# Optimization experiments

Hardware: AMD Instinct MI355X
Metric: run time of the kernel (lower is better)

## Reference

```python
import jax, jax.numpy as jnp
import numpy as np

ALPHA = 1.0


def setup_inputs() -> dict:
    key = jax.random.key(0)
    k1, k2 = jax.random.split(key)
    N, K, D = 131072, 512, 512
    inputs = jax.random.normal(k1, (N, D), dtype=jnp.float32)
    # xavier-uniform style init for clusters
    limit = float(np.sqrt(6.0 / (K + D)))
    clusters = jax.random.uniform(k2, (K, D), dtype=jnp.float32, minval=-limit, maxval=limit)
    return {"inputs": inputs, "clusters": clusters}


def reference(inputs, clusters):
    # (same math as sum((x[:,None,:]-c)**2, -1), without the N x K x D intermediate)
    x2 = jnp.sum(inputs * inputs, axis=1, keepdims=True)          # [N, 1]
    c2 = jnp.sum(clusters * clusters, axis=1)[None, :]            # [1, K]
    d2 = jnp.maximum(x2 + c2 - 2.0 * (inputs @ clusters.T), 0.0)  # [N, K]
    q = 1.0 / (1.0 + d2 / ALPHA)
    q = q ** ((ALPHA + 1.0) / 2.0)
    return q / jnp.sum(q, axis=1, keepdims=True)
```

## Files before the change

kernel.cpp:

```cpp
#include <hip/hip_runtime.h>
#include <stdint.h>

#define NPTS 131072
#define DIM  512
#define KC   512
#define BM   64
#define BK   32
#define NKT  16

typedef float f32x16 __attribute__((ext_vector_type(16)));
typedef float f32x4  __attribute__((ext_vector_type(4)));
typedef short bf16x8 __attribute__((ext_vector_type(8)));
typedef short bf16x4 __attribute__((ext_vector_type(4)));

__device__ __forceinline__ short f2bf(float f) {
  union { float f; unsigned u; } v; v.f = f;
  unsigned r = v.u + 0x7FFFu + ((v.u >> 16) & 1u);
  return (short)(r >> 16);
}

__device__ __forceinline__ bf16x8 pack8(f32x4 a, f32x4 b) {
  bf16x8 p;
  p[0] = f2bf(a.x); p[1] = f2bf(a.y); p[2] = f2bf(a.z); p[3] = f2bf(a.w);
  p[4] = f2bf(b.x); p[5] = f2bf(b.y); p[6] = f2bf(b.z); p[7] = f2bf(b.w);
  return p;
}

__device__ __forceinline__ bf16x4 pack4(f32x4 a) {
  bf16x4 p;
  p[0] = f2bf(a.x); p[1] = f2bf(a.y); p[2] = f2bf(a.z); p[3] = f2bf(a.w);
  return p;
}

__device__ __forceinline__ float sq4(f32x4 a) {
  return a.x*a.x + a.y*a.y + a.z*a.z + a.w*a.w;
}

__device__ __forceinline__ void gload_lds16(const short* g, short* l) {
  __builtin_amdgcn_global_load_lds(
      (const __attribute__((address_space(1))) unsigned int*)g,
      (__attribute__((address_space(3))) unsigned int*)l, 16, 0, 0);
}

__global__ void dec_pack(const float* __restrict__ C, short* __restrict__ Bp,
                         float* __restrict__ c2) {
  const int n    = blockIdx.x;
  const int lane = threadIdx.x;
  const float* src = C + (size_t)n * DIM + lane * 8;
  f32x4 v0 = *(const f32x4*)src;
  f32x4 v1 = *(const f32x4*)(src + 4);
  float s = sq4(v0) + sq4(v1);
  #pragma unroll
  for (int m = 1; m < 64; m <<= 1) s += __shfl_xor(s, m, 64);
  if (lane == 0) c2[n] = s;
  const int kt = lane >> 2;
  const int st = (lane >> 1) & 1;
  const int hh = lane & 1;
  const int wn = n >> 7, nt = (n >> 5) & 3, r = n & 31;
  const size_t slot =
      (((size_t)(kt * 2 + st) * 4 + wn) * 4 + nt) * 64 + hh * 32 + r;
  *(bf16x8*)(Bp + slot * 8) = pack8(v0, v1);
}

__global__ __launch_bounds__(512, 4)
void dec_main(const float* __restrict__ X, const short* __restrict__ Bp,
              const float* __restrict__ c2g, float* __restrict__ out) {
  __shared__ short Bbuf[2][KC * BK];
  __shared__ short Abuf[2][2 * 2 * BM * 8];
  __shared__ float x2sh[BM];
  __shared__ float part[4][BM];
  __shared__ float rowinv[BM];

  const int tid  = threadIdx.x;
  const int lane = tid & 63;
  const int wave = tid >> 6;
  const int wm   = wave >> 2;
  const int wn   = wave & 3;
  const int l31  = lane & 31;
  const int h    = lane >> 5;
  const int row0 = blockIdx.x * BM;

  const int arow = tid >> 3;
  const int ac   = tid & 7;
  const float* aptr = X + (size_t)(row0 + arow) * DIM + ac * 4;
  const int awoff = (((ac >> 2) * 2 + ((ac >> 1) & 1)) * BM + arow) * 8 +
                    (ac & 1) * 4;

  const short* bsrc = Bp + tid * 8;

  f32x16 acc[4];
  #pragma unroll
  for (int nt = 0; nt < 4; ++nt) acc[nt] = (f32x16)0.f;
  float x2a = 0.f;

  {
    #pragma unroll
    for (int sw = 0; sw < 4; ++sw)
      gload_lds16(bsrc + sw * 4096, &Bbuf[0][sw * 4096 + tid * 8]);
    f32x4 a0 = *(const f32x4*)(aptr);
    x2a += sq4(a0);
    *(bf16x4*)&Abuf[0][awoff] = pack4(a0);
  }
  f32x4 av_w = *(const f32x4*)(aptr + 1 * BK);
  f32x4 av_p = *(const f32x4*)(aptr + 2 * BK);
  __syncthreads();

  for (int kt = 0; kt < NKT; ++kt) {
    const int cur = kt & 1, nxt = cur ^ 1;

    if (kt + 1 < NKT) {
      const int kpre = (kt + 3 < NKT) ? (kt + 3) : (NKT - 1);
      f32x4 av_n = *(const f32x4*)(aptr + kpre * BK);
      #pragma unroll
      for (int sw = 0; sw < 4; ++sw)
        gload_lds16(bsrc + (size_t)(kt + 1) * 16384 + sw * 4096,
                    &Bbuf[nxt][sw * 4096 + tid * 8]);
      x2a += sq4(av_w);
      *(bf16x4*)&Abuf[nxt][awoff] = pack4(av_w);
      av_w = av_p;
      av_p = av_n;
    }

    #pragma unroll
    for (int s = 0; s < 2; ++s) {
      bf16x8 af = *(const bf16x8*)
          &Abuf[cur][((s * 2 + h) * BM + wm * 32 + l31) * 8];
      bf16x8 bfr[4];
      #pragma unroll
      for (int nt = 0; nt < 4; ++nt)
        bfr[nt] = *(const bf16x8*)
            &Bbuf[cur][((s * 4 + wn) * 4 + nt) * 512 + lane * 8];
      #pragma unroll
      for (int nt = 0; nt < 4; ++nt)
        acc[nt] = __builtin_amdgcn_mfma_f32_32x32x16_bf16(
            af, bfr[nt], acc[nt], 0, 0, 0);
    }

    __syncthreads();
  }

  x2a += __shfl_xor(x2a, 1, 64);
  x2a += __shfl_xor(x2a, 2, 64);
  x2a += __shfl_xor(x2a, 4, 64);
  if ((tid & 7) == 0) x2sh[arow] = x2a;
  __syncthreads();

  float c2v[4];
  #pragma unroll
  for (int nt = 0; nt < 4; ++nt) c2v[nt] = c2g[wn * 128 + nt * 32 + l31];

  float srow[16];
  #pragma unroll
  for (int r = 0; r < 16; ++r) {
    const int mloc = (r & 3) + 8 * (r >> 2) + 4 * h;
    const float x2m = x2sh[wm * 32 + mloc];
    float s = 0.f;
    #pragma unroll
    for (int nt = 0; nt < 4; ++nt) {
      float d2 = fmaxf(x2m + c2v[nt] - 2.f * acc[nt][r], 0.f);
      float q = __builtin_amdgcn_rcpf(1.f + d2);
      acc[nt][r] = q;
      s += q;
    }
    #pragma unroll
    for (int msk = 1; msk < 32; msk <<= 1) s += __shfl_xor(s, msk, 64);
    srow[r] = s;
  }

  if (l31 == 0) {
    #pragma unroll
    for (int r = 0; r < 16; ++r)
      part[wn][wm * 32 + (r & 3) + 8 * (r >> 2) + 4 * h] = srow[r];
  }
  __syncthreads();
  if (tid < BM)
    rowinv[tid] = __builtin_amdgcn_rcpf(part[0][tid] + part[1][tid] +
                                        part[2][tid] + part[3][tid]);
  __syncthreads();

  #pragma unroll
  for (int r = 0; r < 16; ++r) {
    const int row = wm * 32 + (r & 3) + 8 * (r >> 2) + 4 * h;
    const float iv = rowinv[row];
    float* o = out + (size_t)(row0 + row) * KC + wn * 128 + l31;
    #pragma unroll
    for (int nt = 0; nt < 4; ++nt)
      o[nt * 32] = acc[nt][r] * iv;
  }
}

extern "C" void kernel_launch(void* const* d_in, const int* in_sizes, int n_in,
                              void* d_out, int out_size, void* d_ws, size_t ws_size,
                              hipStream_t stream) {
  const float* X = (const float*)d_in[0];
  const float* C = (const float*)d_in[1];
  float* out = (float*)d_out;

  short* Bp = (short*)d_ws;
  float* c2 = (float*)((char*)d_ws + (size_t)KC * DIM * 2);

  dec_pack<<<KC, 64, 0, stream>>>(C, Bp, c2);
  dec_main<<<NPTS / BM, 512, 0, stream>>>(X, Bp, c2, out);
}
```

Before: 177.5 us.

## Use per-wave private A staging and direct global B loads, removing block barriers

Each wave now loads and converts its own 32-row slice of X into a wave-private LDS double buffer. It also reads packed cluster fragments straight from global memory into registers, so the shared B LDS tile and the per-k-step __syncthreads are gone. Row norms are kept in registers and broadcast with shuffles instead of going through shared memory. The costs are redundant X loads across the four waves that share a wm, more global/L2 traffic for B, more registers, and occupancy lowered to 2 blocks per SM. There is also no wave-level barrier between the LDS write and the read of the next buffer, which relies on in-order wave execution.

```diff
diff --git a/kernel.cpp b/kernel.cpp
--- a/kernel.cpp
+++ b/kernel.cpp
@@ -1,45 +1,44 @@
 #include <hip/hip_runtime.h>
+#include <hip/hip_bf16.h>
 #include <stdint.h>
 
 #define NPTS 131072
 #define DIM  512
 #define KC   512
 #define BM   64
-#define BK   32
 #define NKT  16
 
 typedef float f32x16 __attribute__((ext_vector_type(16)));
 typedef float f32x4  __attribute__((ext_vector_type(4)));
 typedef short bf16x8 __attribute__((ext_vector_type(8)));
-typedef short bf16x4 __attribute__((ext_vector_type(4)));
+
+__device__ __forceinline__ float sq4(f32x4 a) {
+  return a.x*a.x + a.y*a.y + a.z*a.z + a.w*a.w;
+}
+
+__device__ __forceinline__ bf16x8 pack8c(f32x4 a, f32x4 b) {
+  bf16x8 r;
+  float v[8] = {a.x, a.y, a.z, a.w, b.x, b.y, b.z, b.w};
+  #pragma unroll
+  for (int i = 0; i < 4; ++i) {
+    __hip_bfloat162 t = __float22bfloat162_rn(make_float2(v[2*i], v[2*i+1]));
+    union { __hip_bfloat162 h; short s[2]; } u; u.h = t;
+    r[2*i]   = u.s[0];
+    r[2*i+1] = u.s[1];
+  }
+  return r;
+}
 
 __device__ __forceinline__ short f2bf(float f) {
   union { float f; unsigned u; } v; v.f = f;
   unsigned r = v.u + 0x7FFFu + ((v.u >> 16) & 1u);
   return (short)(r >> 16);
 }
-
 __device__ __forceinline__ bf16x8 pack8(f32x4 a, f32x4 b) {
   bf16x8 p;
   p[0] = f2bf(a.x); p[1] = f2bf(a.y); p[2] = f2bf(a.z); p[3] = f2bf(a.w);
   p[4] = f2bf(b.x); p[5] = f2bf(b.y); p[6] = f2bf(b.z); p[7] = f2bf(b.w);
   return p;
-}
-
-__device__ __forceinline__ bf16x4 pack4(f32x4 a) {
-  bf16x4 p;
-  p[0] = f2bf(a.x); p[1] = f2bf(a.y); p[2] = f2bf(a.z); p[3] = f2bf(a.w);
-  return p;
-}
-
-__device__ __forceinline__ float sq4(f32x4 a) {
-  return a.x*a.x + a.y*a.y + a.z*a.z + a.w*a.w;
-}
-
-__device__ __forceinline__ void gload_lds16(const short* g, short* l) {
-  __builtin_amdgcn_global_load_lds(
-      (const __attribute__((address_space(1))) unsigned int*)g,
-      (__attribute__((address_space(3))) unsigned int*)l, 16, 0, 0);
 }
 
 __global__ void dec_pack(const float* __restrict__ C, short* __restrict__ Bp,
@@ -62,12 +61,10 @@
   *(bf16x8*)(Bp + slot * 8) = pack8(v0, v1);
 }
 
-__global__ __launch_bounds__(512, 4)
+__global__ __launch_bounds__(512, 2)
 void dec_main(const float* __restrict__ X, const short* __restrict__ Bp,
               const float* __restrict__ c2g, float* __restrict__ out) {
-  __shared__ short Bbuf[2][KC * BK];
-  __shared__ short Abuf[2][2 * 2 * BM * 8];
-  __shared__ float x2sh[BM];
+  __shared__ short Apriv[8][2][1024];
   __shared__ float part[4][BM];
   __shared__ float rowinv[BM];
 
@@ -80,70 +77,86 @@
   const int h    = lane >> 5;
   const int row0 = blockIdx.x * BM;
 
-  const int arow = tid >> 3;
-  const int ac   = tid & 7;
-  const float* aptr = X + (size_t)(row0 + arow) * DIM + ac * 4;
-  const int awoff = (((ac >> 2) * 2 + ((ac >> 1) & 1)) * BM + arow) * 8 +
-                    (ac & 1) * 4;
-
-  const short* bsrc = Bp + tid * 8;
+  const float* aptr =
+      X + (size_t)(row0 + wm * 32 + (lane >> 2)) * DIM + (lane & 3) * 8;
+  const short* bB = Bp + wn * 2048 + lane * 8;
+  const int awoff = (lane & 3) * 256 + (lane >> 2) * 8;
 
   f32x16 acc[4];
   #pragma unroll
   for (int nt = 0; nt < 4; ++nt) acc[nt] = (f32x16)0.f;
-  float x2a = 0.f;
+  float x2s[2] = {0.f, 0.f};
 
   {
-    #pragma unroll
-    for (int sw = 0; sw < 4; ++sw)
-      gload_lds16(bsrc + sw * 4096, &Bbuf[0][sw * 4096 + tid * 8]);
-    f32x4 a0 = *(const f32x4*)(aptr);
-    x2a += sq4(a0);
-    *(bf16x4*)&Abuf[0][awoff] = pack4(a0);
-  }
-  f32x4 av_w = *(const f32x4*)(aptr + 1 * BK);
-  f32x4 av_p = *(const f32x4*)(aptr + 2 * BK);
-  __syncthreads();
-
+    f32x4 a0[2][2];
+    #pragma unroll
+    for (int j = 0; j < 2; ++j) {
+      a0[j][0] = *(const f32x4*)(aptr + j * 8192);
+      a0[j][1] = *(const f32x4*)(aptr + j * 8192 + 4);
+    }
+    #pragma unroll
+    for (int j = 0; j < 2; ++j) {
+      x2s[j] += sq4(a0[j][0]) + sq4(a0[j][1]);
+      *(bf16x8*)&Apriv[wave][0][awoff + j * 128] = pack8c(a0[j][0], a0[j][1]);
+    }
+  }
+  f32x4 aC[2][2];
+  #pragma unroll
+  for (int j = 0; j < 2; ++j) {
+    aC[j][0] = *(const f32x4*)(aptr + 32 + j * 8192);
+    aC[j][1] = *(const f32x4*)(aptr + 32 + j * 8192 + 4);
+  }
+
+  #pragma unroll 2
   for (int kt = 0; kt < NKT; ++kt) {
-    const int cur = kt & 1, nxt = cur ^ 1;
+    const int cur = kt & 1;
+
+    f32x4 aN[2][2];
+    if (kt + 2 < NKT) {
+      #pragma unroll
+      for (int j = 0; j < 2; ++j) {
+        aN[j][0] = *(const f32x4*)(aptr + (kt + 2) * 32 + j * 8192);
+        aN[j][1] = *(const f32x4*)(aptr + (kt + 2) * 32 + j * 8192 + 4);
+      }
+    }
+
+    bf16x8 bq[2][4];
+    #pragma unroll
+    for (int s = 0; s < 2; ++s)
+      #pragma unroll
+      for (int nt = 0; nt < 4; ++nt)
+        bq[s][nt] = *(const bf16x8*)(bB + kt * 16384 + s * 8192 + nt * 512);
 
     if (kt + 1 < NKT) {
-      const int kpre = (kt + 3 < NKT) ? (kt + 3) : (NKT - 1);
-      f32x4 av_n = *(const f32x4*)(aptr + kpre * BK);
-      #pragma unroll
-      for (int sw = 0; sw < 4; ++sw)
-        gload_lds16(bsrc + (size_t)(kt + 1) * 16384 + sw * 4096,
-                    &Bbuf[nxt][sw * 4096 + tid * 8]);
-      x2a += sq4(av_w);
-      *(bf16x4*)&Abuf[nxt][awoff] = pack4(av_w);
-      av_w = av_p;
-      av_p = av_n;
+      #pragma unroll
+      for (int j = 0; j < 2; ++j) {
+        x2s[j] += sq4(aC[j][0]) + sq4(aC[j][1]);
+        *(bf16x8*)&Apriv[wave][cur ^ 1][awoff + j * 128] =
+            pack8c(aC[j][0], aC[j][1]);
+      }
     }
 
     #pragma unroll
     for (int s = 0; s < 2; ++s) {
-      bf16x8 af = *(const bf16x8*)
-          &Abuf[cur][((s * 2 + h) * BM + wm * 32 + l31) * 8];
-      bf16x8 bfr[4];
-      #pragma unroll
-      for (int nt = 0; nt < 4; ++nt)
-        bfr[nt] = *(const bf16x8*)
-            &Bbuf[cur][((s * 4 + wn) * 4 + nt) * 512 + lane * 8];
+      bf16x8 af = *(const bf16x8*)&Apriv[wave][cur][(s * 2 + h) * 256 + l31 * 8];
       #pragma unroll
       for (int nt = 0; nt < 4; ++nt)
         acc[nt] = __builtin_amdgcn_mfma_f32_32x32x16_bf16(
-            af, bfr[nt], acc[nt], 0, 0, 0);
-    }
-
-    __syncthreads();
-  }
-
-  x2a += __shfl_xor(x2a, 1, 64);
-  x2a += __shfl_xor(x2a, 2, 64);
-  x2a += __shfl_xor(x2a, 4, 64);
-  if ((tid & 7) == 0) x2sh[arow] = x2a;
-  __syncthreads();
+            af, bq[s][nt], acc[nt], 0, 0, 0);
+    }
+
+    #pragma unroll
+    for (int j = 0; j < 2; ++j) {
+      aC[j][0] = aN[j][0];
+      aC[j][1] = aN[j][1];
+    }
+  }
+
+  #pragma unroll
+  for (int j = 0; j < 2; ++j) {
+    x2s[j] += __shfl_xor(x2s[j], 1, 64);
+    x2s[j] += __shfl_xor(x2s[j], 2, 64);
+  }
 
   float c2v[4];
   #pragma unroll
@@ -153,7 +166,7 @@
   #pragma unroll
   for (int r = 0; r < 16; ++r) {
     const int mloc = (r & 3) + 8 * (r >> 2) + 4 * h;
-    const float x2m = x2sh[wm * 32 + mloc];
+    const float x2m = __shfl(x2s[mloc >> 4], (mloc & 15) * 4, 64);
     float s = 0.f;
     #pragma unroll
     for (int nt = 0; nt < 4; ++nt) {
```

Result: slower. 216.0 us (+21.7%).

## Pre-pack inputs to bf16 MFMA layout and drop LDS staging in main GEMM

Applied to the files above, without the earlier changes.

Adds a separate kernel that converts X to bf16 in the MFMA fragment layout and computes row norms. The main kernel then reads A and B fragments directly from global memory into registers, with no LDS double buffering or barriers in the k-loop. This is meant to remove LDS traffic and synchronisation from the GEMM loop. The cost is an extra pass over X, a large bf16 workspace write, and more global/L2 reads of B per wave. The old kernel is kept as a fallback when the workspace is too small.

```diff
diff --git a/kernel.cpp b/kernel.cpp
--- a/kernel.cpp
+++ b/kernel.cpp
@@ -1,45 +1,44 @@
 #include <hip/hip_runtime.h>
+#include <hip/hip_bf16.h>
 #include <stdint.h>
 
 #define NPTS 131072
 #define DIM  512
 #define KC   512
 #define BM   64
-#define BK   32
 #define NKT  16
 
 typedef float f32x16 __attribute__((ext_vector_type(16)));
 typedef float f32x4  __attribute__((ext_vector_type(4)));
 typedef short bf16x8 __attribute__((ext_vector_type(8)));
-typedef short bf16x4 __attribute__((ext_vector_type(4)));
+
+__device__ __forceinline__ float sq4(f32x4 a) {
+  return a.x*a.x + a.y*a.y + a.z*a.z + a.w*a.w;
+}
+
+__device__ __forceinline__ bf16x8 pack8c(f32x4 a, f32x4 b) {
+  bf16x8 r;
+  float v[8] = {a.x, a.y, a.z, a.w, b.x, b.y, b.z, b.w};
+  #pragma unroll
+  for (int i = 0; i < 4; ++i) {
+    __hip_bfloat162 t = __float22bfloat162_rn(make_float2(v[2*i], v[2*i+1]));
+    union { __hip_bfloat162 h; short s[2]; } u; u.h = t;
+    r[2*i]   = u.s[0];
+    r[2*i+1] = u.s[1];
+  }
+  return r;
+}
 
 __device__ __forceinline__ short f2bf(float f) {
   union { float f; unsigned u; } v; v.f = f;
   unsigned r = v.u + 0x7FFFu + ((v.u >> 16) & 1u);
   return (short)(r >> 16);
 }
-
 __device__ __forceinline__ bf16x8 pack8(f32x4 a, f32x4 b) {
   bf16x8 p;
   p[0] = f2bf(a.x); p[1] = f2bf(a.y); p[2] = f2bf(a.z); p[3] = f2bf(a.w);
   p[4] = f2bf(b.x); p[5] = f2bf(b.y); p[6] = f2bf(b.z); p[7] = f2bf(b.w);
   return p;
-}
-
-__device__ __forceinline__ bf16x4 pack4(f32x4 a) {
-  bf16x4 p;
-  p[0] = f2bf(a.x); p[1] = f2bf(a.y); p[2] = f2bf(a.z); p[3] = f2bf(a.w);
-  return p;
-}
-
-__device__ __forceinline__ float sq4(f32x4 a) {
-  return a.x*a.x + a.y*a.y + a.z*a.z + a.w*a.w;
-}
-
-__device__ __forceinline__ void gload_lds16(const short* g, short* l) {
-  __builtin_amdgcn_global_load_lds(
-      (const __attribute__((address_space(1))) unsigned int*)g,
-      (__attribute__((address_space(3))) unsigned int*)l, 16, 0, 0);
 }
 
 __global__ void dec_pack(const float* __restrict__ C, short* __restrict__ Bp,
@@ -62,12 +61,31 @@
   *(bf16x8*)(Bp + slot * 8) = pack8(v0, v1);
 }
 
-__global__ __launch_bounds__(512, 4)
-void dec_main(const float* __restrict__ X, const short* __restrict__ Bp,
-              const float* __restrict__ c2g, float* __restrict__ out) {
-  __shared__ short Bbuf[2][KC * BK];
-  __shared__ short Abuf[2][2 * 2 * BM * 8];
-  __shared__ float x2sh[BM];
+__global__ __launch_bounds__(256)
+void dec_packx(const float* __restrict__ X, short* __restrict__ Xp,
+               float* __restrict__ x2g) {
+  const int g    = blockIdx.x * 4 + (threadIdx.x >> 6);
+  const int lane = threadIdx.x & 63;
+  const int h    = lane >> 5;
+  const int r    = lane & 31;
+  const float* src = X + (size_t)(g * 32 + r) * DIM + h * 8;
+  short* dst = Xp + (size_t)g * 16384 + lane * 8;
+  float x2 = 0.f;
+  #pragma unroll 4
+  for (int ks = 0; ks < 32; ++ks) {
+    f32x4 lo = *(const f32x4*)(src + ks * 16);
+    f32x4 hi = *(const f32x4*)(src + ks * 16 + 4);
+    x2 += sq4(lo) + sq4(hi);
+    *(bf16x8*)(dst + ks * 512) = pack8c(lo, hi);
+  }
+  x2 += __shfl_xor(x2, 32, 64);
+  if (lane < 32) x2g[g * 32 + r] = x2;
+}
+
+__global__ __launch_bounds__(512)
+void dec_main2(const short* __restrict__ Xp, const short* __restrict__ Bp,
+               const float* __restrict__ c2g, const float* __restrict__ x2g,
+               float* __restrict__ out) {
   __shared__ float part[4][BM];
   __shared__ float rowinv[BM];
 
@@ -79,13 +97,124 @@
   const int l31  = lane & 31;
   const int h    = lane >> 5;
   const int row0 = blockIdx.x * BM;
+  const int g    = blockIdx.x * 2 + wm;
+
+  const short* aB = Xp + (size_t)g * 16384 + lane * 8;
+  const short* bB = Bp + wn * 2048 + lane * 8;
+
+  f32x16 acc[4];
+  #pragma unroll
+  for (int nt = 0; nt < 4; ++nt) acc[nt] = (f32x16)0.f;
+
+  bf16x8 aF[2][2];
+  #pragma unroll
+  for (int s = 0; s < 2; ++s)
+    aF[0][s] = *(const bf16x8*)(aB + s * 512);
+
+  #pragma unroll
+  for (int kt = 0; kt < NKT; ++kt) {
+    bf16x8 bF[2][4];
+    #pragma unroll
+    for (int s = 0; s < 2; ++s)
+      #pragma unroll
+      for (int nt = 0; nt < 4; ++nt)
+        bF[s][nt] = *(const bf16x8*)(bB + kt * 16384 + s * 8192 + nt * 512);
+
+    if (kt + 1 < NKT) {
+      #pragma unroll
+      for (int s = 0; s < 2; ++s)
+        aF[(kt + 1) & 1][s] =
+            *(const bf16x8*)(aB + (kt + 1) * 1024 + s * 512);
+    }
+
+    #pragma unroll
+    for (int s = 0; s < 2; ++s)
+      #pragma unroll
+      for (int nt = 0; nt < 4; ++nt)
+        acc[nt] = __builtin_amdgcn_mfma_f32_32x32x16_bf16(
+            aF[kt & 1][s], bF[s][nt], acc[nt], 0, 0, 0);
+  }
+
+  const float x2v = x2g[row0 + wm * 32 + l31];
+  float c2v[4];
+  #pragma unroll
+  for (int nt = 0; nt < 4; ++nt) c2v[nt] = c2g[wn * 128 + nt * 32 + l31];
+
+  float srow[16];
+  #pragma unroll
+  for (int r = 0; r < 16; ++r) {
+    const int mloc = (r & 3) + 8 * (r >> 2) + 4 * h;
+    const float x2m = __shfl(x2v, mloc, 64);
+    float s = 0.f;
+    #pragma unroll
+    for (int nt = 0; nt < 4; ++nt) {
+      float d2 = fmaxf(x2m + c2v[nt] - 2.f * acc[nt][r], 0.f);
+      float q = __builtin_amdgcn_rcpf(1.f + d2);
+      acc[nt][r] = q;
+      s += q;
+    }
+    #pragma unroll
+    for (int msk = 1; msk < 32; msk <<= 1) s += __shfl_xor(s, msk, 64);
+    srow[r] = s;
+  }
+
+  if (l31 == 0) {
+    #pragma unroll
+    for (int r = 0; r < 16; ++r)
+      part[wn][wm * 32 + (r & 3) + 8 * (r >> 2) + 4 * h] = srow[r];
+  }
+  __syncthreads();
+  if (tid < BM)
+    rowinv[tid] = __builtin_amdgcn_rcpf(part[0][tid] + part[1][tid] +
+                                        part[2][tid] + part[3][tid]);
+  __syncthreads();
+
+  #pragma unroll
+  for (int r = 0; r < 16; ++r) {
+    const int row = wm * 32 + (r & 3) + 8 * (r >> 2) + 4 * h;
+    const float iv = rowinv[row];
+    float* o = out + (size_t)(row0 + row) * KC + wn * 128 + l31;
+    #pragma unroll
+    for (int nt = 0; nt < 4; ++nt)
+      o[nt * 32] = acc[nt][r] * iv;
+  }
+}
+
+typedef short bf16x4 __attribute__((ext_vector_type(4)));
+__device__ __forceinline__ bf16x4 pack4(f32x4 a) {
+  bf16x4 p;
+  p[0] = f2bf(a.x); p[1] = f2bf(a.y); p[2] = f2bf(a.z); p[3] = f2bf(a.w);
+  return p;
+}
+__device__ __forceinline__ void gload_lds16(const short* g, short* l) {
+  __builtin_amdgcn_global_load_lds(
+      (const __attribute__((address_space(1))) unsigned int*)g,
+      (__attribute__((address_space(3))) unsigned int*)l, 16, 0, 0);
+}
+
+__global__ __launch_bounds__(512, 4)
+void dec_main_fb(const float* __restrict__ X, const short* __restrict__ Bp,
+                 const float* __restrict__ c2g, float* __restrict__ out) {
+  __shared__ short Bbuf[2][KC * 32];
+  __shared__ short Abuf[2][2 * 2 * BM * 8];
+  __shared__ float x2sh[BM];
+  __shared__ float part[4][BM];
+  __shared__ float rowinv[BM];
+
+  const int tid  = threadIdx.x;
+  const int lane = tid & 63;
+  const int wave = tid >> 6;
+  const int wm   = wave >> 2;
+  const int wn   = wave & 3;
+  const int l31  = lane & 31;
+  const int h    = lane >> 5;
+  const int row0 = blockIdx.x * BM;
 
   const int arow = tid >> 3;
   const int ac   = tid & 7;
   const float* aptr = X + (size_t)(row0 + arow) * DIM + ac * 4;
   const int awoff = (((ac >> 2) * 2 + ((ac >> 1) & 1)) * BM + arow) * 8 +
                     (ac & 1) * 4;
-
   const short* bsrc = Bp + tid * 8;
 
   f32x16 acc[4];
@@ -101,16 +230,15 @@
     x2a += sq4(a0);
     *(bf16x4*)&Abuf[0][awoff] = pack4(a0);
   }
-  f32x4 av_w = *(const f32x4*)(aptr + 1 * BK);
-  f32x4 av_p = *(const f32x4*)(aptr + 2 * BK);
+  f32x4 av_w = *(const f32x4*)(aptr + 32);
+  f32x4 av_p = *(const f32x4*)(aptr + 64);
   __syncthreads();
 
   for (int kt = 0; kt < NKT; ++kt) {
     const int cur = kt & 1, nxt = cur ^ 1;
-
     if (kt + 1 < NKT) {
       const int kpre = (kt + 3 < NKT) ? (kt + 3) : (NKT - 1);
-      f32x4 av_n = *(const f32x4*)(aptr + kpre * BK);
+      f32x4 av_n = *(const f32x4*)(aptr + kpre * 32);
       #pragma unroll
       for (int sw = 0; sw < 4; ++sw)
         gload_lds16(bsrc + (size_t)(kt + 1) * 16384 + sw * 4096,
@@ -120,7 +248,6 @@
       av_w = av_p;
       av_p = av_n;
     }
-
     #pragma unroll
     for (int s = 0; s < 2; ++s) {
       bf16x8 af = *(const bf16x8*)
@@ -135,7 +262,6 @@
         acc[nt] = __builtin_amdgcn_mfma_f32_32x32x16_bf16(
             af, bfr[nt], acc[nt], 0, 0, 0);
     }
-
     __syncthreads();
   }
 
@@ -166,7 +292,6 @@
     for (int msk = 1; msk < 32; msk <<= 1) s += __shfl_xor(s, msk, 64);
     srow[r] = s;
   }
-
   if (l31 == 0) {
     #pragma unroll
     for (int r = 0; r < 16; ++r)
@@ -177,7 +302,6 @@
     rowinv[tid] = __builtin_amdgcn_rcpf(part[0][tid] + part[1][tid] +
                                         part[2][tid] + part[3][tid]);
   __syncthreads();
-
   #pragma unroll
   for (int r = 0; r < 16; ++r) {
     const int row = wm * 32 + (r & 3) + 8 * (r >> 2) + 4 * h;
@@ -196,9 +320,18 @@
   const float* C = (const float*)d_in[1];
   float* out = (float*)d_out;
 
-  short* Bp = (short*)d_ws;
-  float* c2 = (float*)((char*)d_ws + (size_t)KC * DIM * 2);
+  char* ws = (char*)d_ws;
+  short* Bp  = (short*)ws;
+  float* c2  = (float*)(ws + (size_t)KC * DIM * 2);
+  float* x2g = (float*)(ws + (size_t)KC * DIM * 2 + 4096);
+  short* Xp  = (short*)(ws + (1u << 21));
+  const size_t REQ = (1u << 21) + (size_t)NPTS * DIM * 2;
 
   dec_pack<<<KC, 64, 0, stream>>>(C, Bp, c2);
-  dec_main<<<NPTS / BM, 512, 0, stream>>>(X, Bp, c2, out);
-}
+  if (ws_size >= REQ) {
+    dec_packx<<<NPTS / 128, 256, 0, stream>>>(X, Xp, x2g);
+    dec_main2<<<NPTS / BM, 512, 0, stream>>>(Xp, Bp, c2, x2g, out);
+  } else {
+    dec_main_fb<<<NPTS / BM, 512, 0, stream>>>(X, Bp, c2, out);
+  }
+}
```

Result: slower. 272.8 us (+53.7%).

## Load fp32 X tiles into LDS asynchronously and convert to bf16 after LDS read

Applied to the files above, without the earlier changes.

The X tile is no longer loaded into registers, converted to bf16 and written to LDS. Raw fp32 rows are now copied straight into a swizzled LDS buffer with global_load_lds, and each wave converts its A fragment to bf16 (via __float22bfloat162_rn) right before the MFMA. Row norms are now accumulated from the LDS fragments and spread with shuffles instead of a shared-memory reduction. The launch-bounds occupancy hint is also dropped. This takes the register-staged prefetch and its VALU packing off the load path, but doubles A's LDS footprint and repeats the conversion in every wave sharing a row tile.

```diff
diff --git a/kernel.cpp b/kernel.cpp
--- a/kernel.cpp
+++ b/kernel.cpp
@@ -1,4 +1,5 @@
 #include <hip/hip_runtime.h>
+#include <hip/hip_bf16.h>
 #include <stdint.h>
 
 #define NPTS 131072
@@ -11,14 +12,29 @@
 typedef float f32x16 __attribute__((ext_vector_type(16)));
 typedef float f32x4  __attribute__((ext_vector_type(4)));
 typedef short bf16x8 __attribute__((ext_vector_type(8)));
-typedef short bf16x4 __attribute__((ext_vector_type(4)));
+
+__device__ __forceinline__ float sq4(f32x4 a) {
+  return a.x*a.x + a.y*a.y + a.z*a.z + a.w*a.w;
+}
+
+__device__ __forceinline__ bf16x8 pack8c(f32x4 a, f32x4 b) {
+  bf16x8 r;
+  float v[8] = {a.x, a.y, a.z, a.w, b.x, b.y, b.z, b.w};
+  #pragma unroll
+  for (int i = 0; i < 4; ++i) {
+    __hip_bfloat162 t = __float22bfloat162_rn(make_float2(v[2*i], v[2*i+1]));
+    union { __hip_bfloat162 h; short s[2]; } u; u.h = t;
+    r[2*i]   = u.s[0];
+    r[2*i+1] = u.s[1];
+  }
+  return r;
+}
 
 __device__ __forceinline__ short f2bf(float f) {
   union { float f; unsigned u; } v; v.f = f;
   unsigned r = v.u + 0x7FFFu + ((v.u >> 16) & 1u);
   return (short)(r >> 16);
 }
-
 __device__ __forceinline__ bf16x8 pack8(f32x4 a, f32x4 b) {
   bf16x8 p;
   p[0] = f2bf(a.x); p[1] = f2bf(a.y); p[2] = f2bf(a.z); p[3] = f2bf(a.w);
@@ -26,17 +42,7 @@
   return p;
 }
 
-__device__ __forceinline__ bf16x4 pack4(f32x4 a) {
-  bf16x4 p;
-  p[0] = f2bf(a.x); p[1] = f2bf(a.y); p[2] = f2bf(a.z); p[3] = f2bf(a.w);
-  return p;
-}
-
-__device__ __forceinline__ float sq4(f32x4 a) {
-  return a.x*a.x + a.y*a.y + a.z*a.z + a.w*a.w;
-}
-
-__device__ __forceinline__ void gload_lds16(const short* g, short* l) {
+__device__ __forceinline__ void gload_lds16(const void* g, void* l) {
   __builtin_amdgcn_global_load_lds(
       (const __attribute__((address_space(1))) unsigned int*)g,
       (__attribute__((address_space(3))) unsigned int*)l, 16, 0, 0);
@@ -62,14 +68,11 @@
   *(bf16x8*)(Bp + slot * 8) = pack8(v0, v1);
 }
 
-__global__ __launch_bounds__(512, 4)
+__global__ __launch_bounds__(512)
 void dec_main(const float* __restrict__ X, const short* __restrict__ Bp,
               const float* __restrict__ c2g, float* __restrict__ out) {
   __shared__ short Bbuf[2][KC * BK];
-  __shared__ short Abuf[2][2 * 2 * BM * 8];
-  __shared__ float x2sh[BM];
-  __shared__ float part[4][BM];
-  __shared__ float rowinv[BM];
+  __shared__ float Abuf[2][BM * BK];
 
   const int tid  = threadIdx.x;
   const int lane = tid & 63;
@@ -80,51 +83,42 @@
   const int h    = lane >> 5;
   const int row0 = blockIdx.x * BM;
 
-  const int arow = tid >> 3;
-  const int ac   = tid & 7;
-  const float* aptr = X + (size_t)(row0 + arow) * DIM + ac * 4;
-  const int awoff = (((ac >> 2) * 2 + ((ac >> 1) & 1)) * BM + arow) * 8 +
-                    (ac & 1) * 4;
+  const float* asrc = X + (size_t)(row0 + (tid >> 3)) * DIM +
+                      (((tid & 7) ^ ((tid >> 3) & 7)) << 2);
+  const short* bsrc = Bp + tid * 8;
 
-  const short* bsrc = Bp + tid * 8;
+  const int arow = (wm * 32 + l31) * BK;
 
   f32x16 acc[4];
   #pragma unroll
   for (int nt = 0; nt < 4; ++nt) acc[nt] = (f32x16)0.f;
-  float x2a = 0.f;
+  float x2 = 0.f;
 
-  {
-    #pragma unroll
-    for (int sw = 0; sw < 4; ++sw)
-      gload_lds16(bsrc + sw * 4096, &Bbuf[0][sw * 4096 + tid * 8]);
-    f32x4 a0 = *(const f32x4*)(aptr);
-    x2a += sq4(a0);
-    *(bf16x4*)&Abuf[0][awoff] = pack4(a0);
-  }
-  f32x4 av_w = *(const f32x4*)(aptr + 1 * BK);
-  f32x4 av_p = *(const f32x4*)(aptr + 2 * BK);
+  #pragma unroll
+  for (int sw = 0; sw < 4; ++sw)
+    gload_lds16(bsrc + sw * 4096, &Bbuf[0][sw * 4096 + tid * 8]);
+  gload_lds16(asrc, &Abuf[0][tid * 4]);
   __syncthreads();
 
   for (int kt = 0; kt < NKT; ++kt) {
     const int cur = kt & 1, nxt = cur ^ 1;
 
     if (kt + 1 < NKT) {
-      const int kpre = (kt + 3 < NKT) ? (kt + 3) : (NKT - 1);
-      f32x4 av_n = *(const f32x4*)(aptr + kpre * BK);
       #pragma unroll
       for (int sw = 0; sw < 4; ++sw)
         gload_lds16(bsrc + (size_t)(kt + 1) * 16384 + sw * 4096,
                     &Bbuf[nxt][sw * 4096 + tid * 8]);
-      x2a += sq4(av_w);
-      *(bf16x4*)&Abuf[nxt][awoff] = pack4(av_w);
-      av_w = av_p;
-      av_p = av_n;
+      gload_lds16(asrc + (kt + 1) * BK, &Abuf[nxt][tid * 4]);
     }
 
     #pragma unroll
     for (int s = 0; s < 2; ++s) {
-      bf16x8 af = *(const bf16x8*)
-          &Abuf[cur][((s * 2 + h) * BM + wm * 32 + l31) * 8];
+      f32x4 lo = *(const f32x4*)
+          &Abuf[cur][arow + (((s * 4 + h * 2 + 0) ^ (l31 & 7)) << 2)];
+      f32x4 hi = *(const f32x4*)
+          &Abuf[cur][arow + (((s * 4 + h * 2 + 1) ^ (l31 & 7)) << 2)];
+      x2 += sq4(lo) + sq4(hi);
+      bf16x8 af = pack8c(lo, hi);
       bf16x8 bfr[4];
       #pragma unroll
       for (int nt = 0; nt < 4; ++nt)
@@ -139,11 +133,7 @@
     __syncthreads();
   }
 
-  x2a += __shfl_xor(x2a, 1, 64);
-  x2a += __shfl_xor(x2a, 2, 64);
-  x2a += __shfl_xor(x2a, 4, 64);
-  if ((tid & 7) == 0) x2sh[arow] = x2a;
-  __syncthreads();
+  x2 += __shfl_xor(x2, 32, 64);
 
   float c2v[4];
   #pragma unroll
@@ -153,7 +143,7 @@
   #pragma unroll
   for (int r = 0; r < 16; ++r) {
     const int mloc = (r & 3) + 8 * (r >> 2) + 4 * h;
-    const float x2m = x2sh[wm * 32 + mloc];
+    const float x2m = __shfl(x2, mloc, 64);
     float s = 0.f;
     #pragma unroll
     for (int nt = 0; nt < 4; ++nt) {
@@ -167,15 +157,18 @@
     srow[r] = s;
   }
 
+  float* part   = &Abuf[0][0];
+  float* rowinv = &Abuf[0][4 * BM];
+
   if (l31 == 0) {
     #pragma unroll
     for (int r = 0; r < 16; ++r)
-      part[wn][wm * 32 + (r & 3) + 8 * (r >> 2) + 4 * h] = srow[r];
+      part[wn * BM + wm * 32 + (r & 3) + 8 * (r >> 2) + 4 * h] = srow[r];
   }
   __syncthreads();
   if (tid < BM)
-    rowinv[tid] = __builtin_amdgcn_rcpf(part[0][tid] + part[1][tid] +
-                                        part[2][tid] + part[3][tid]);
+    rowinv[tid] = __builtin_amdgcn_rcpf(part[tid] + part[BM + tid] +
+                                        part[2 * BM + tid] + part[3 * BM + tid]);
   __syncthreads();
 
   #pragma unroll
```

Result: slower. 227.9 us (+28.4%).
